# Kernel tuning notes

Hardware: AMD Instinct MI355X
Metric: run time of the kernel (lower is better)

Reference implementation:

```python
import jax, jax.numpy as jnp
import numpy as np

TF_ALPHA = 0.125  # teacher-forcing blend used in forward()


def setup_inputs() -> dict:
    key = jax.random.key(0)
    ks = jax.random.split(key, 6)
    B, T, dx, dz, dy = 512, 1024, 32, 64, 256
    return {
        "X": jax.random.normal(ks[0], (B, T, dx), dtype=jnp.float32),
        "A": (jax.random.normal(ks[1], (dz,), dtype=jnp.float32) * 0.1),
        "W1": jax.random.normal(ks[2], (dz, dy), dtype=jnp.float32) / np.sqrt(dy).astype(np.float32),
        "W2": jax.random.normal(ks[3], (dy, dz), dtype=jnp.float32) / np.sqrt(dz).astype(np.float32),
        "h1": jax.random.normal(ks[4], (dz,), dtype=jnp.float32) * 0.01,
        "h2": jax.random.normal(ks[5], (dy,), dtype=jnp.float32) * 0.01,
    }


def reference(X, A, W1, W2, h1, h2):
    # X: (batch, time, dim_x); shallow-PLRNN, dim_x_proj=0, no mean centering, no inputs.
    B, T, dx = X.shape
    dz = A.shape[0]

    def teacher_force(z, f, alpha):
        # blend forcing signal into first dx latent dims where f is not NaN
        blend = alpha * f + (1.0 - alpha) * z[:, :dx]
        return z.at[:, :dx].set(jnp.where(jnp.isnan(f), z[:, :dx], blend))

    # z0 = teacher_force(zeros, X[:,0], alpha=1)
    z0 = teacher_force(jnp.zeros((B, dz), X.dtype), X[:, 0], 1.0)

    Xt = jnp.transpose(X, (1, 0, 2))  # (T, B, dx)

    def step(z, x_t):
        zf = teacher_force(z, x_t, TF_ALPHA)
        # shallow-PLRNN: z' = A*z + W1 @ relu(W2 @ z + h2) + h1
        hidden = jax.nn.relu(jnp.einsum('yz,bz->by', W2, zf) + h2)
        z_new = A * zf + jnp.einsum('zy,by->bz', W1, hidden) + h1
        return z_new, z_new

    _, Z = jax.lax.scan(step, z0, Xt)          # (T, B, dz)
    Z = jnp.transpose(Z, (1, 0, 2))            # (B, T, dz)
    return Z[:, :, :dx]                        # output = first dim_x latent dims
```

## Files before the change

kernel.cpp:

```cpp
#include <hip/hip_runtime.h>

#define BB 512
#define TT 1024
#define DX 32
#define DZ 64
#define DY 256
#define ALPHA 0.125f
#define HP 36

template<int CTRL>
__device__ __forceinline__ float dpp_add(float x) {
    int p = __builtin_amdgcn_update_dpp(0, __float_as_int(x), CTRL, 0xF, 0xF, true);
    return x + __int_as_float(p);
}

__global__ __launch_bounds__(512, 4)
void plrnn_scan(const float* __restrict__ X, const float* __restrict__ A,
                const float* __restrict__ W1, const float* __restrict__ W2,
                const float* __restrict__ h1, const float* __restrict__ h2,
                float* __restrict__ out) {
    const int b   = blockIdx.x;
    const int tid = threadIdx.x;

    const int y    = tid >> 1;
    const int half = tid & 1;
    const int z    = tid >> 3;
    const int oct  = tid & 7;
    const int wv   = tid >> 6;

    __shared__ float zf_s[DZ];
    __shared__ float hid_s[8 * HP];

    float4 w2r[8];
    float4 w1r[8];
#pragma unroll
    for (int j = 0; j < 8; ++j) {
        w2r[j] = *(const float4*)&W2[y * DZ + 32 * half + 4 * j];
        w1r[j] = *(const float4*)&W1[z * DY + 32 * oct + 4 * j];
    }
#pragma unroll
    for (int j = 0; j < 8; ++j) {
        asm volatile("" : "+v"(w2r[j].x), "+v"(w2r[j].y),
                          "+v"(w2r[j].z), "+v"(w2r[j].w));
        asm volatile("" : "+v"(w1r[j].x), "+v"(w1r[j].y),
                          "+v"(w1r[j].z), "+v"(w1r[j].w));
    }

    float h2init = (half == 0) ? h2[y] : 0.0f;
    float h1init = (oct == 0) ? h1[z] : 0.0f;
    float Ar     = A[z];
    asm volatile("" : "+v"(h2init), "+v"(h1init), "+v"(Ar));

    const bool zdx = (z < DX);

    const float* xp = X   + (size_t)b * TT * DX + z;
    float*       op = out + (size_t)b * TT * DX + z;

    float zfr = 0.0f;
    if (zdx) { float x0 = xp[0]; zfr = (x0 == x0) ? x0 : 0.0f; }
    if (oct == 0) zf_s[z] = zfr;
    __syncthreads();

    const int hidx = wv * HP + (y & 31);

    auto step = [&](const int koff, const int pfoff) {
        float xnext = 0.0f;
        if (zdx) xnext = xp[pfoff];

        const float4* zp = (const float4*)(zf_s + 32 * half);
        float a0 = h2init, a1 = 0.f, a2 = 0.f, a3 = 0.f;
#pragma unroll
        for (int j = 0; j < 8; ++j) {
            float4 v = zp[j];
            a0 = fmaf(w2r[j].x, v.x, a0);
            a1 = fmaf(w2r[j].y, v.y, a1);
            a2 = fmaf(w2r[j].z, v.z, a2);
            a3 = fmaf(w2r[j].w, v.w, a3);
        }
        float d1 = (a0 + a1) + (a2 + a3);
        d1 = dpp_add<0xB1>(d1);
        if (half == 0) hid_s[hidx] = fmaxf(d1, 0.0f);
        __syncthreads();

        const float4* hp = (const float4*)(hid_s + HP * oct);
        float p0 = h1init, p1 = 0.f, p2 = 0.f, p3 = 0.f;
#pragma unroll
        for (int j = 0; j < 8; ++j) {
            float4 v = hp[j];
            p0 = fmaf(w1r[j].x, v.x, p0);
            p1 = fmaf(w1r[j].y, v.y, p1);
            p2 = fmaf(w1r[j].z, v.z, p2);
            p3 = fmaf(w1r[j].w, v.w, p3);
        }
        float d2 = (p0 + p1) + (p2 + p3);
        d2 = dpp_add<0xB1>(d2);
        d2 = dpp_add<0x4E>(d2);
        d2 = dpp_add<0x141>(d2);

        float zn = fmaf(Ar, zfr, d2);
        if (zdx) {
            if (oct == 0) op[koff * DX] = zn;
            zfr = (xnext == xnext) ? fmaf(ALPHA, xnext, 0.875f * zn) : zn;
        } else {
            zfr = zn;
        }
        if (oct == 0) zf_s[z] = zfr;
        __syncthreads();
    };

    for (int tg = 0; tg < TT - 8; tg += 8) {
#pragma unroll
        for (int k = 0; k < 8; ++k) step(k, (k + 1) * DX);
        xp += 8 * DX;
        op += 8 * DX;
    }
#pragma unroll
    for (int k = 0; k < 8; ++k) step(k, (k < 7 ? (k + 1) : 7) * DX);
}

extern "C" void kernel_launch(void* const* d_in, const int* in_sizes, int n_in,
                              void* d_out, int out_size, void* d_ws, size_t ws_size,
                              hipStream_t stream) {
    const float* X  = (const float*)d_in[0];
    const float* A  = (const float*)d_in[1];
    const float* W1 = (const float*)d_in[2];
    const float* W2 = (const float*)d_in[3];
    const float* h1 = (const float*)d_in[4];
    const float* h2 = (const float*)d_in[5];
    float* out = (float*)d_out;

    plrnn_scan<<<BB, 512, 0, stream>>>(X, A, W1, W2, h1, h2, out);
}
```

Before: 918.0 us.

## Remap thread work to cut LDS traffic per recurrent step

Changes how work is split across threads. For W2 @ z, each 8-lane group now computes four hidden outputs from an 8-wide z slice and reduces with DPP. For W1 @ hidden, each 16-lane group computes two latent outputs over a 16-wide hidden slice. The goal is fewer shared-memory reads per FMA, with padded LDS rows to avoid bank conflicts. It also drops the 8-step unrolled loop in favour of a single-step loop that prefetches x one step ahead, and it adds more DPP reduction steps.

```diff
diff --git a/kernel.cpp b/kernel.cpp
--- a/kernel.cpp
+++ b/kernel.cpp
@@ -6,7 +6,6 @@
 #define DZ 64
 #define DY 256
 #define ALPHA 0.125f
-#define HP 36
 
 template<int CTRL>
 __device__ __forceinline__ float dpp_add(float x) {
@@ -14,7 +13,8 @@
     return x + __int_as_float(p);
 }
 
-__global__ __launch_bounds__(512, 4)
+__global__ __launch_bounds__(512)
+__attribute__((amdgpu_waves_per_eu(4, 4)))
 void plrnn_scan(const float* __restrict__ X, const float* __restrict__ A,
                 const float* __restrict__ W1, const float* __restrict__ W2,
                 const float* __restrict__ h1, const float* __restrict__ h2,
@@ -22,100 +22,139 @@
     const int b   = blockIdx.x;
     const int tid = threadIdx.x;
 
-    const int y    = tid >> 1;
-    const int half = tid & 1;
-    const int z    = tid >> 3;
-    const int oct  = tid & 7;
-    const int wv   = tid >> 6;
+    const int g   = tid >> 3;
+    const int oct = tid & 7;
+    const int g2  = tid >> 4;
+    const int l16 = tid & 15;
 
     __shared__ float zf_s[DZ];
-    __shared__ float hid_s[8 * HP];
+    __shared__ float hid_s[DY + (DY / 16) * 4];
 
     float4 w2r[8];
-    float4 w1r[8];
 #pragma unroll
-    for (int j = 0; j < 8; ++j) {
-        w2r[j] = *(const float4*)&W2[y * DZ + 32 * half + 4 * j];
-        w1r[j] = *(const float4*)&W1[z * DY + 32 * oct + 4 * j];
+    for (int k = 0; k < 8; ++k) {
+        const int col = 8 * oct + k;
+        w2r[k] = make_float4(W2[(4 * g + 0) * DZ + col], W2[(4 * g + 1) * DZ + col],
+                             W2[(4 * g + 2) * DZ + col], W2[(4 * g + 3) * DZ + col]);
     }
+    float4 wa[4], wb[4];
 #pragma unroll
-    for (int j = 0; j < 8; ++j) {
-        asm volatile("" : "+v"(w2r[j].x), "+v"(w2r[j].y),
-                          "+v"(w2r[j].z), "+v"(w2r[j].w));
-        asm volatile("" : "+v"(w1r[j].x), "+v"(w1r[j].y),
-                          "+v"(w1r[j].z), "+v"(w1r[j].w));
+    for (int j = 0; j < 4; ++j) {
+        wa[j] = *(const float4*)&W1[(2 * g2 + 0) * DY + 16 * l16 + 4 * j];
+        wb[j] = *(const float4*)&W1[(2 * g2 + 1) * DY + 16 * l16 + 4 * j];
     }
+    float4 h2i = make_float4(0.f, 0.f, 0.f, 0.f);
+    if (oct == 0) h2i = *(const float4*)&h2[4 * g];
+    float h1a = 0.f, h1b = 0.f;
+    if (l16 == 0) { h1a = h1[2 * g2]; h1b = h1[2 * g2 + 1]; }
+    const float2 Av = *(const float2*)&A[2 * g2];
 
-    float h2init = (half == 0) ? h2[y] : 0.0f;
-    float h1init = (oct == 0) ? h1[z] : 0.0f;
-    float Ar     = A[z];
-    asm volatile("" : "+v"(h2init), "+v"(h1init), "+v"(Ar));
+#pragma unroll
+    for (int k = 0; k < 8; ++k)
+        asm volatile("" : "+v"(w2r[k].x), "+v"(w2r[k].y),
+                          "+v"(w2r[k].z), "+v"(w2r[k].w));
+#pragma unroll
+    for (int j = 0; j < 4; ++j) {
+        asm volatile("" : "+v"(wa[j].x), "+v"(wa[j].y), "+v"(wa[j].z), "+v"(wa[j].w));
+        asm volatile("" : "+v"(wb[j].x), "+v"(wb[j].y), "+v"(wb[j].z), "+v"(wb[j].w));
+    }
+    asm volatile("" : "+v"(h2i.x), "+v"(h2i.y), "+v"(h2i.z), "+v"(h2i.w));
 
-    const bool zdx = (z < DX);
+    const bool zdx = (g2 < 16);
 
-    const float* xp = X   + (size_t)b * TT * DX + z;
-    float*       op = out + (size_t)b * TT * DX + z;
+    const float* xq = X   + (size_t)b * TT * DX + 2 * g2;
+    float*       op = out + (size_t)b * TT * DX + 2 * g2;
 
-    float zfr = 0.0f;
-    if (zdx) { float x0 = xp[0]; zfr = (x0 == x0) ? x0 : 0.0f; }
-    if (oct == 0) zf_s[z] = zfr;
+    const int hwr = 4 * g + ((4 * g) >> 4) * 4;
+    const int hrd = 20 * l16;
+
+    float zf0 = 0.f, zf1 = 0.f;
+    if (zdx) {
+        const float2 x0 = *(const float2*)xq;
+        zf0 = (x0.x == x0.x) ? x0.x : 0.f;
+        zf1 = (x0.y == x0.y) ? x0.y : 0.f;
+    }
+    if (l16 == 0) *(float2*)&zf_s[2 * g2] = make_float2(zf0, zf1);
     __syncthreads();
+    xq += DX;
 
-    const int hidx = wv * HP + (y & 31);
-
-    auto step = [&](const int koff, const int pfoff) {
-        float xnext = 0.0f;
-        if (zdx) xnext = xp[pfoff];
-
-        const float4* zp = (const float4*)(zf_s + 32 * half);
-        float a0 = h2init, a1 = 0.f, a2 = 0.f, a3 = 0.f;
+    auto step = [&](const float2 xn) {
+        float zl[8];
+        {
+            const float4* zp = (const float4*)(zf_s + 8 * oct);
+            *(float4*)&zl[0] = zp[0];
+            *(float4*)&zl[4] = zp[1];
+        }
+        float ax = h2i.x, ay = h2i.y, az = h2i.z, aw = h2i.w;
 #pragma unroll
-        for (int j = 0; j < 8; ++j) {
-            float4 v = zp[j];
-            a0 = fmaf(w2r[j].x, v.x, a0);
-            a1 = fmaf(w2r[j].y, v.y, a1);
-            a2 = fmaf(w2r[j].z, v.z, a2);
-            a3 = fmaf(w2r[j].w, v.w, a3);
+        for (int k = 0; k < 8; ++k) {
+            ax = fmaf(w2r[k].x, zl[k], ax);
+            ay = fmaf(w2r[k].y, zl[k], ay);
+            az = fmaf(w2r[k].z, zl[k], az);
+            aw = fmaf(w2r[k].w, zl[k], aw);
         }
-        float d1 = (a0 + a1) + (a2 + a3);
-        d1 = dpp_add<0xB1>(d1);
-        if (half == 0) hid_s[hidx] = fmaxf(d1, 0.0f);
+        ax = dpp_add<0xB1>(ax); ay = dpp_add<0xB1>(ay);
+        az = dpp_add<0xB1>(az); aw = dpp_add<0xB1>(aw);
+        ax = dpp_add<0x4E>(ax); ay = dpp_add<0x4E>(ay);
+        az = dpp_add<0x4E>(az); aw = dpp_add<0x4E>(aw);
+        ax = dpp_add<0x141>(ax); ay = dpp_add<0x141>(ay);
+        az = dpp_add<0x141>(az); aw = dpp_add<0x141>(aw);
+        if (oct == 0)
+            *(float4*)&hid_s[hwr] = make_float4(fmaxf(ax, 0.f), fmaxf(ay, 0.f),
+                                                fmaxf(az, 0.f), fmaxf(aw, 0.f));
         __syncthreads();
 
-        const float4* hp = (const float4*)(hid_s + HP * oct);
-        float p0 = h1init, p1 = 0.f, p2 = 0.f, p3 = 0.f;
+        float hl[16];
+        {
+            const float4* hp = (const float4*)(hid_s + hrd);
+            *(float4*)&hl[0]  = hp[0];
+            *(float4*)&hl[4]  = hp[1];
+            *(float4*)&hl[8]  = hp[2];
+            *(float4*)&hl[12] = hp[3];
+        }
+        float p0 = h1a, p1 = 0.f, q0 = h1b, q1 = 0.f;
 #pragma unroll
-        for (int j = 0; j < 8; ++j) {
-            float4 v = hp[j];
-            p0 = fmaf(w1r[j].x, v.x, p0);
-            p1 = fmaf(w1r[j].y, v.y, p1);
-            p2 = fmaf(w1r[j].z, v.z, p2);
-            p3 = fmaf(w1r[j].w, v.w, p3);
+        for (int j = 0; j < 4; ++j) {
+            p0 = fmaf(wa[j].x, hl[4 * j + 0], p0);
+            p1 = fmaf(wa[j].y, hl[4 * j + 1], p1);
+            p0 = fmaf(wa[j].z, hl[4 * j + 2], p0);
+            p1 = fmaf(wa[j].w, hl[4 * j + 3], p1);
+            q0 = fmaf(wb[j].x, hl[4 * j + 0], q0);
+            q1 = fmaf(wb[j].y, hl[4 * j + 1], q1);
+            q0 = fmaf(wb[j].z, hl[4 * j + 2], q0);
+            q1 = fmaf(wb[j].w, hl[4 * j + 3], q1);
         }
-        float d2 = (p0 + p1) + (p2 + p3);
-        d2 = dpp_add<0xB1>(d2);
-        d2 = dpp_add<0x4E>(d2);
-        d2 = dpp_add<0x141>(d2);
+        float d0 = p0 + p1, d1 = q0 + q1;
+        d0 = dpp_add<0xB1>(d0);  d1 = dpp_add<0xB1>(d1);
+        d0 = dpp_add<0x4E>(d0);  d1 = dpp_add<0x4E>(d1);
+        d0 = dpp_add<0x141>(d0); d1 = dpp_add<0x141>(d1);
+        d0 = dpp_add<0x140>(d0); d1 = dpp_add<0x140>(d1);
 
-        float zn = fmaf(Ar, zfr, d2);
+        const float zn0 = fmaf(Av.x, zf0, d0);
+        const float zn1 = fmaf(Av.y, zf1, d1);
         if (zdx) {
-            if (oct == 0) op[koff * DX] = zn;
-            zfr = (xnext == xnext) ? fmaf(ALPHA, xnext, 0.875f * zn) : zn;
+            if (l16 == 0) *(float2*)op = make_float2(zn0, zn1);
+            zf0 = (xn.x == xn.x) ? fmaf(ALPHA, xn.x, 0.875f * zn0) : zn0;
+            zf1 = (xn.y == xn.y) ? fmaf(ALPHA, xn.y, 0.875f * zn1) : zn1;
         } else {
-            zfr = zn;
+            zf0 = zn0;
+            zf1 = zn1;
         }
-        if (oct == 0) zf_s[z] = zfr;
+        if (l16 == 0) *(float2*)&zf_s[2 * g2] = make_float2(zf0, zf1);
         __syncthreads();
     };
 
-    for (int tg = 0; tg < TT - 8; tg += 8) {
-#pragma unroll
-        for (int k = 0; k < 8; ++k) step(k, (k + 1) * DX);
-        xp += 8 * DX;
-        op += 8 * DX;
+    for (int t = 0; t < TT - 1; ++t) {
+        float2 xn = make_float2(0.f, 0.f);
+        if (zdx) xn = *(const float2*)xq;
+        xq += DX;
+        step(xn);
+        op += DX;
     }
-#pragma unroll
-    for (int k = 0; k < 8; ++k) step(k, (k < 7 ? (k + 1) : 7) * DX);
+    {
+        const float nanf_ = __int_as_float(0x7fc00000);
+        step(make_float2(nanf_, nanf_));
+    }
 }
 
 extern "C" void kernel_launch(void* const* d_in, const int* in_sizes, int n_in,
```

Result: faster. 833.7 us (-9.2%).

## Restructure PLRNN step to one barrier per step with per-wave redundant state

Applied to the files above, without the earlier changes.

Each wave now computes 32 hidden units and a partial W1 product for all 64 latent dims. The partials go to double-buffered shared memory, and after a single barrier every wave redundantly reduces them and keeps its own copy of the latent state. This removes one of the two block-wide barriers per time step, plus the cross-lane DPP reductions for the second matvec, at the cost of more shared-memory reads and redundant reduction work in every wave. X prefetch is simplified to two steps ahead, and the asm register pinning is removed.

```diff
diff --git a/kernel.cpp b/kernel.cpp
--- a/kernel.cpp
+++ b/kernel.cpp
@@ -6,69 +6,56 @@
 #define DZ 64
 #define DY 256
 #define ALPHA 0.125f
-#define HP 36
+#define PS 68
 
-template<int CTRL>
-__device__ __forceinline__ float dpp_add(float x) {
-    int p = __builtin_amdgcn_update_dpp(0, __float_as_int(x), CTRL, 0xF, 0xF, true);
+__device__ __forceinline__ float dpp_add_xor1(float x) {
+    int p = __builtin_amdgcn_update_dpp(0, __float_as_int(x), 0xB1, 0xF, 0xF, true);
     return x + __int_as_float(p);
 }
 
-__global__ __launch_bounds__(512, 4)
+__global__ __launch_bounds__(512)
+__attribute__((amdgpu_waves_per_eu(4, 4)))
 void plrnn_scan(const float* __restrict__ X, const float* __restrict__ A,
                 const float* __restrict__ W1, const float* __restrict__ W2,
                 const float* __restrict__ h1, const float* __restrict__ h2,
                 float* __restrict__ out) {
     const int b   = blockIdx.x;
     const int tid = threadIdx.x;
+    const int l   = tid & 63;
+    const int w   = tid >> 6;
+    const int r   = l >> 1;
+    const int h   = l & 1;
+    const int y   = 32 * w + r;
 
-    const int y    = tid >> 1;
-    const int half = tid & 1;
-    const int z    = tid >> 3;
-    const int oct  = tid & 7;
-    const int wv   = tid >> 6;
-
-    __shared__ float zf_s[DZ];
-    __shared__ float hid_s[8 * HP];
+    __shared__ float zf_s[8][DZ];
+    __shared__ float hid_s[8][32];
+    __shared__ float part_s[2][8 * PS];
 
     float4 w2r[8];
     float4 w1r[8];
 #pragma unroll
     for (int j = 0; j < 8; ++j) {
-        w2r[j] = *(const float4*)&W2[y * DZ + 32 * half + 4 * j];
-        w1r[j] = *(const float4*)&W1[z * DY + 32 * oct + 4 * j];
+        w2r[j] = *(const float4*)&W2[y * DZ + 32 * h + 4 * j];
+        w1r[j] = *(const float4*)&W1[l * DY + 32 * w + 4 * j];
     }
-#pragma unroll
-    for (int j = 0; j < 8; ++j) {
-        asm volatile("" : "+v"(w2r[j].x), "+v"(w2r[j].y),
-                          "+v"(w2r[j].z), "+v"(w2r[j].w));
-        asm volatile("" : "+v"(w1r[j].x), "+v"(w1r[j].y),
-                          "+v"(w1r[j].z), "+v"(w1r[j].w));
-    }
+    const float h2i = (h == 0) ? h2[y] : 0.0f;
+    const float Al  = A[l];
+    const float h1l = h1[l];
 
-    float h2init = (half == 0) ? h2[y] : 0.0f;
-    float h1init = (oct == 0) ? h1[z] : 0.0f;
-    float Ar     = A[z];
-    asm volatile("" : "+v"(h2init), "+v"(h1init), "+v"(Ar));
+    const float* Xb = X   + (size_t)b * TT * DX;
+    float*       Ob = out + (size_t)b * TT * DX;
 
-    const bool zdx = (z < DX);
+    float zfreg = 0.0f;
+    if (l < DX) { float x0 = Xb[l]; zfreg = (x0 == x0) ? x0 : 0.0f; }
+    zf_s[w][l] = zfreg;
 
-    const float* xp = X   + (size_t)b * TT * DX + z;
-    float*       op = out + (size_t)b * TT * DX + z;
+    const float* xq = Xb + l + DX;
+    float*       oq = Ob + l;
+    const float  NANF = __int_as_float(0x7fc00000);
 
-    float zfr = 0.0f;
-    if (zdx) { float x0 = xp[0]; zfr = (x0 == x0) ? x0 : 0.0f; }
-    if (oct == 0) zf_s[z] = zfr;
-    __syncthreads();
-
-    const int hidx = wv * HP + (y & 31);
-
-    auto step = [&](const int koff, const int pfoff) {
-        float xnext = 0.0f;
-        if (zdx) xnext = xp[pfoff];
-
-        const float4* zp = (const float4*)(zf_s + 32 * half);
-        float a0 = h2init, a1 = 0.f, a2 = 0.f, a3 = 0.f;
+    auto step = [&](float* pbuf, const float xn, const int tOff) {
+        const float4* zp = (const float4*)&zf_s[w][32 * h];
+        float a0 = h2i, a1 = 0.f, a2 = 0.f, a3 = 0.f;
 #pragma unroll
         for (int j = 0; j < 8; ++j) {
             float4 v = zp[j];
@@ -78,12 +65,11 @@
             a3 = fmaf(w2r[j].w, v.w, a3);
         }
         float d1 = (a0 + a1) + (a2 + a3);
-        d1 = dpp_add<0xB1>(d1);
-        if (half == 0) hid_s[hidx] = fmaxf(d1, 0.0f);
-        __syncthreads();
+        d1 = dpp_add_xor1(d1);
+        if (h == 0) hid_s[w][r] = fmaxf(d1, 0.0f);
 
-        const float4* hp = (const float4*)(hid_s + HP * oct);
-        float p0 = h1init, p1 = 0.f, p2 = 0.f, p3 = 0.f;
+        const float4* hp = (const float4*)&hid_s[w][0];
+        float p0 = 0.f, p1 = 0.f, p2 = 0.f, p3 = 0.f;
 #pragma unroll
         for (int j = 0; j < 8; ++j) {
             float4 v = hp[j];
@@ -92,30 +78,29 @@
             p2 = fmaf(w1r[j].z, v.z, p2);
             p3 = fmaf(w1r[j].w, v.w, p3);
         }
-        float d2 = (p0 + p1) + (p2 + p3);
-        d2 = dpp_add<0xB1>(d2);
-        d2 = dpp_add<0x4E>(d2);
-        d2 = dpp_add<0x141>(d2);
+        pbuf[w * PS + l] = (p0 + p1) + (p2 + p3);
 
-        float zn = fmaf(Ar, zfr, d2);
-        if (zdx) {
-            if (oct == 0) op[koff * DX] = zn;
-            zfr = (xnext == xnext) ? fmaf(ALPHA, xnext, 0.875f * zn) : zn;
-        } else {
-            zfr = zn;
-        }
-        if (oct == 0) zf_s[z] = zfr;
         __syncthreads();
+
+        const float* ps = pbuf + l;
+        float s = ((ps[0 * PS] + ps[1 * PS]) + (ps[2 * PS] + ps[3 * PS])) +
+                  ((ps[4 * PS] + ps[5 * PS]) + (ps[6 * PS] + ps[7 * PS]));
+        float zn = fmaf(Al, zfreg, s + h1l);
+        if (w == 0 && l < DX) oq[tOff] = zn;
+        zfreg = (xn == xn) ? fmaf(ALPHA, xn, (1.0f - ALPHA) * zn) : zn;
+        zf_s[w][l] = zfreg;
     };
 
-    for (int tg = 0; tg < TT - 8; tg += 8) {
-#pragma unroll
-        for (int k = 0; k < 8; ++k) step(k, (k + 1) * DX);
-        xp += 8 * DX;
-        op += 8 * DX;
+    for (int t = 0; t < TT; t += 2) {
+        float xn0 = NANF, xn1 = NANF;
+        if (l < DX) {
+            xn0 = xq[0];
+            if (t + 2 < TT) xn1 = xq[DX];
+        }
+        xq += 2 * DX;
+        step(&part_s[0][0], xn0, t * DX);
+        step(&part_s[1][0], xn1, (t + 1) * DX);
     }
-#pragma unroll
-    for (int k = 0; k < 8; ++k) step(k, (k < 7 ? (k + 1) : 7) * DX);
 }
 
 extern "C" void kernel_launch(void* const* d_in, const int* in_sizes, int n_in,
```

After: 941.4 us. 1.03x slower.
